# Optimization experiments

Measured on AMD Instinct MI355X. Metric: run time of the kernel, lower is better.

Reference implementation:

```python
import jax, jax.numpy as jnp
import numpy as np

INV_SQRT2 = 0.7071067811865476  # Haar (db1) filter coefficient


def _haar_wavedec(x, level):
    """Haar (db1) multi-level DWT along axis=2 of x: [B,H,L,Dh].
    Returns [cA_n, cD_n, cD_{n-1}, ..., cD_1] (pywt.wavedec ordering).
    Exact match to pywt for L divisible by 2**level (no boundary padding needed)."""
    details = []
    a = x
    for _ in range(level):
        e, o = a[:, :, 0::2, :], a[:, :, 1::2, :]
        details.append((e - o) * INV_SQRT2)
        a = (e + o) * INV_SQRT2
    return [a] + details[::-1]


def _haar_idwt_step(a, d):
    """Single-level Haar inverse DWT along axis=2."""
    e = (a + d) * INV_SQRT2
    o = (a - d) * INV_SQRT2
    B, H, Lh, Dh = a.shape
    return jnp.stack([e, o], axis=3).reshape(B, H, 2 * Lh, Dh)


def setup_inputs() -> dict:
    key = jax.random.key(0)
    ks = jax.random.split(key, 6)
    B, L, D, H, M = 8, 4096, 1024, 16, 3
    Dh = D // H
    return {
        "query": jax.random.normal(ks[0], (B, L, D), jnp.float32),
        "W_qkv": jax.random.normal(ks[1], (3 * D, D), jnp.float32) * 0.02,
        "b_qkv": jnp.zeros((3 * D,), jnp.float32),
        "W_out": jax.random.normal(ks[2], (D, D), jnp.float32) * 0.02,
        "b_out": jnp.zeros((D,), jnp.float32),
        "weight_q": jax.random.normal(ks[3], (H, M, Dh), jnp.float32),
        "weight_v": jax.random.normal(ks[4], (H, M, Dh), jnp.float32),
    }


def reference(query, W_qkv, b_qkv, W_out, b_out, weight_q, weight_v):
    B, L, D = query.shape
    H, M, Dh = weight_q.shape  # n_heads, modes, head_dim

    qkv = query @ W_qkv.T + b_qkv               # [B,L,3D]; k chunk is unused (as in original)
    q = qkv[..., :D].reshape(B, L, H, Dh).transpose(0, 2, 1, 3)      # [B,H,L,Dh]
    v = qkv[..., 2 * D:].reshape(B, L, H, Dh).transpose(0, 2, 1, 3)  # [B,H,L,Dh]

    cq = _haar_wavedec(q, M)  # [cA_M, cD_M, ..., cD_1]
    cv = _haar_wavedec(v, M)

    # Weight the coarsest `modes` bands per head/channel, then multiply q*v in wavelet domain.
    prod = []
    for j in range(M):
        wq = weight_q[None, :, j, None, :]  # [1,H,1,Dh]
        wv = weight_v[None, :, j, None, :]
        prod.append((cq[j] * wq) * (cv[j] * wv))
    prod.append(cq[M] * cv[M])  # finest detail band, unweighted

    # Inverse DWT back to length L.
    a = prod[0]
    for d in prod[1:]:
        a = _haar_idwt_step(a, d)

    out = a.transpose(0, 2, 1, 3).reshape(B, L, D)
    return out @ W_out.T + b_out  # dropout is identity in eval
```

## Files before the change

kernel.cpp:

```cpp
#include <hip/hip_runtime.h>
#include <hip/hip_fp16.h>
#include <cstdint>
#include <cstddef>

typedef _Float16 f16;
typedef __attribute__((ext_vector_type(4))) _Float16 f16x4;
typedef __attribute__((ext_vector_type(8))) _Float16 f16x8;
typedef __attribute__((ext_vector_type(4))) float f32x4;

#define C_INV_SQRT2 0.70710678118654752440f

__device__ __forceinline__ void gld_lds16(const void* g, void* l) {
  __builtin_amdgcn_global_load_lds((const __attribute__((address_space(1))) void*)g,
                                   (__attribute__((address_space(3))) void*)l, 16, 0, 0);
}

__global__ __launch_bounds__(256) void cvt_f32_f16_k(const float* __restrict__ in,
                                                     f16* __restrict__ out, int n4) {
  int i = blockIdx.x * 256 + threadIdx.x;
  if (i >= n4) return;
  const float4 x = ((const float4*)in)[i];
  f16x4 y;
  y.x = (f16)x.x; y.y = (f16)x.y; y.z = (f16)x.z; y.w = (f16)x.w;
  ((f16x4*)out)[i] = y;
}

__global__ __launch_bounds__(256) void pack_wqv_k(const float* __restrict__ W,
                                                  const float* __restrict__ b,
                                                  f16* __restrict__ Wo,
                                                  float* __restrict__ bo) {
  int i = blockIdx.x * 256 + threadIdx.x;
  int n = i >> 8;
  int c = (i & 255) * 4;
  int sn = (n < 1024) ? n : (n + 1024);
  const float4 x = *(const float4*)(W + (size_t)sn * 1024 + c);
  f16x4 y; y.x = (f16)x.x; y.y = (f16)x.y; y.z = (f16)x.z; y.w = (f16)x.w;
  *(f16x4*)(Wo + (size_t)n * 1024 + c) = y;
  if (i < 2048) bo[i] = b[(i < 1024) ? i : (i + 1024)];
}

__device__ __forceinline__ void haar_mid(const f16x8 q8, const f16x8 v8,
                                         float wq0, float wq1, float wq2,
                                         float wv0, float wv1, float wv2,
                                         float* a8) {
  const float c = C_INV_SQRT2;
  float q[8], v[8];
#pragma unroll
  for (int i = 0; i < 8; i++) { q[i] = (float)q8[i]; v[i] = (float)v8[i]; }
  float qa1[4], qd1[4], va1[4], vd1[4];
#pragma unroll
  for (int i = 0; i < 4; i++) {
    qd1[i] = (q[2 * i] - q[2 * i + 1]) * c;
    qa1[i] = (q[2 * i] + q[2 * i + 1]) * c;
    vd1[i] = (v[2 * i] - v[2 * i + 1]) * c;
    va1[i] = (v[2 * i] + v[2 * i + 1]) * c;
  }
  float qa2[2], qd2[2], va2[2], vd2[2];
#pragma unroll
  for (int j = 0; j < 2; j++) {
    qd2[j] = (qa1[2 * j] - qa1[2 * j + 1]) * c;
    qa2[j] = (qa1[2 * j] + qa1[2 * j + 1]) * c;
    vd2[j] = (va1[2 * j] - va1[2 * j + 1]) * c;
    va2[j] = (va1[2 * j] + va1[2 * j + 1]) * c;
  }
  const float qd3 = (qa2[0] - qa2[1]) * c, qa3 = (qa2[0] + qa2[1]) * c;
  const float vd3 = (va2[0] - va2[1]) * c, va3 = (va2[0] + va2[1]) * c;
  const float pa = (qa3 * wq0) * (va3 * wv0);
  const float pd3 = (qd3 * wq1) * (vd3 * wv1);
  float pd2[2], pd1[4];
#pragma unroll
  for (int j = 0; j < 2; j++) pd2[j] = (qd2[j] * wq2) * (vd2[j] * wv2);
#pragma unroll
  for (int i = 0; i < 4; i++) pd1[i] = qd1[i] * vd1[i];
  float s2[2], s1[4];
  s2[0] = (pa + pd3) * c;
  s2[1] = (pa - pd3) * c;
#pragma unroll
  for (int j = 0; j < 2; j++) {
    s1[2 * j] = (s2[j] + pd2[j]) * c;
    s1[2 * j + 1] = (s2[j] - pd2[j]) * c;
  }
#pragma unroll
  for (int i = 0; i < 4; i++) {
    a8[2 * i] = (s1[i] + pd1[i]) * c;
    a8[2 * i + 1] = (s1[i] - pd1[i]) * c;
  }
}


#define STAGEH(bufi, mat, half, Gbase, k0)                         \
  {                                                                \
    f16* Ld = &lds[bufi][mat][half][0];                            \
    const f16* Gp = (Gbase) + (size_t)srow * K + (k0) + sch * 8;   \
    gld_lds16(Gp, Ld + (w * 64) * 8);                              \
    gld_lds16(Gp + (size_t)64 * K, Ld + (4096 + w * 64 * 8));      \
  }

#define MFMA_PH(mi0)                                                             \
  __builtin_amdgcn_s_setprio(1);                                                 \
  _Pragma("unroll") for (int mm = (mi0); mm < (mi0) + 2; mm++)                   \
      _Pragma("unroll") for (int nj = 0; nj < 4; nj++) {                         \
    acc[mm][nj] = __builtin_amdgcn_mfma_f32_16x16x32_f16(aF[mm][0], bF[nj][0],   \
                                                         acc[mm][nj], 0, 0, 0);  \
    acc[mm][nj] = __builtin_amdgcn_mfma_f32_16x16x32_f16(aF[mm][1], bF[nj][1],   \
                                                         acc[mm][nj], 0, 0, 0);  \
  }                                                                              \
  __builtin_amdgcn_s_setprio(0);

#define BAR_SEQ()                       \
  __builtin_amdgcn_sched_barrier(0);    \
  __builtin_amdgcn_s_barrier();         \
  __builtin_amdgcn_sched_barrier(0);

template <typename CT, bool FUSED>
__global__ __launch_bounds__(512, 2) void gemm256_k(const f16* __restrict__ A,
                                                    const f16* __restrict__ B,
                                                    const float* __restrict__ bias,
                                                    CT* __restrict__ C,
                                                    const float* __restrict__ wq,
                                                    const float* __restrict__ wv,
                                                    int M, int N, int K, int nbx) {
  __shared__ f16 lds[2][2][2][128 * 64];
  const int t = threadIdx.x;
  const int w = t >> 6, l = t & 63;
  const int wm = w >> 2, wn = w & 3;
  const int hi = l >> 4, lo = l & 15;

  const int nwg = gridDim.x;
  const int cpx = nwg >> 3;
  const int bid = blockIdx.x;
  const int nid = (bid & 7) * cpx + (bid >> 3);
  const int by = nid / nbx, bx = nid - by * nbx;
  const int m0 = by * 256;
  const int n0 = bx * 256;
  const int d0 = bx * 128;

  const f16* GA = A + (size_t)m0 * K;
  const f16* GBq = FUSED ? (B + (size_t)d0 * K) : (B + (size_t)n0 * K);
  const f16* GBv = FUSED ? (B + (size_t)(1024 + d0) * K) : (GBq + (size_t)128 * K);

  const int srow = t >> 3;
  const int sch = (t & 7) ^ (srow & 7);

  const int colk0 = ((hi ^ (lo & 7)) << 3);
  const int colk1 = (((4 | hi) ^ (lo & 7)) << 3);

  f32x4 acc[8][4] = {};
  f16x8 aF[8][2], bF[4][2];
  const int NT = K >> 6;

  STAGEH(0, 0, 0, GA, 0); STAGEH(0, 0, 1, GA + (size_t)128 * K, 0);
  STAGEH(0, 1, 0, GBq, 0); STAGEH(0, 1, 1, GBv, 0);
  STAGEH(1, 0, 0, GA, 64); STAGEH(1, 0, 1, GA + (size_t)128 * K, 64);

  for (int tt = 0; tt < NT; ++tt) {
    const int buf = tt & 1;
    const f16* pA = &lds[buf][0][wm][0] + lo * 64;
    const f16* pB = &lds[buf][1][wn >> 1][0] + (wn & 1) * 4096 + lo * 64;
    const f16* pA0 = pA + colk0;
    const f16* pA1 = pA + colk1;
    const f16* pB0 = pB + colk0;
    const f16* pB1 = pB + colk1;

    if (tt < NT - 1) {
      asm volatile("s_waitcnt vmcnt(4)" ::: "memory");
    } else {
      asm volatile("s_waitcnt vmcnt(0)" ::: "memory");
    }
    BAR_SEQ();
    aF[0][0] = *(const f16x8*)(pA0 + 0 * 1024);
    aF[0][1] = *(const f16x8*)(pA1 + 0 * 1024);
    aF[1][0] = *(const f16x8*)(pA0 + 1 * 1024);
    aF[1][1] = *(const f16x8*)(pA1 + 1 * 1024);
#pragma unroll
    for (int nj = 0; nj < 4; nj++) {
      bF[nj][0] = *(const f16x8*)(pB0 + nj * 1024);
      bF[nj][1] = *(const f16x8*)(pB1 + nj * 1024);
    }
    aF[2][0] = *(const f16x8*)(pA0 + 2 * 1024);
    aF[2][1] = *(const f16x8*)(pA1 + 2 * 1024);
    aF[3][0] = *(const f16x8*)(pA0 + 3 * 1024);
    aF[3][1] = *(const f16x8*)(pA1 + 3 * 1024);
    if (tt + 1 < NT) STAGEH(buf ^ 1, 1, 0, GBq, (tt + 1) * 64);
    MFMA_PH(0);

    BAR_SEQ();
#pragma unroll
    for (int mi = 4; mi < 8; mi++) {
      aF[mi][0] = *(const f16x8*)(pA0 + mi * 1024);
      aF[mi][1] = *(const f16x8*)(pA1 + mi * 1024);
    }
    if (tt + 1 < NT) STAGEH(buf ^ 1, 1, 1, GBv, (tt + 1) * 64);
    MFMA_PH(2);

    asm volatile("s_waitcnt lgkmcnt(0)" ::: "memory");
    BAR_SEQ();
    if (tt + 2 < NT) STAGEH(buf, 0, 0, GA, (tt + 2) * 64);
    MFMA_PH(4);

    asm volatile("s_waitcnt lgkmcnt(0)" ::: "memory");
    BAR_SEQ();
    if (tt + 2 < NT) STAGEH(buf, 0, 1, GA + (size_t)128 * K, (tt + 2) * 64);
    MFMA_PH(6);
  }

  if (!FUSED) {
#pragma unroll
    for (int mi = 0; mi < 8; mi++) {
#pragma unroll
      for (int nj = 0; nj < 4; nj++) {
        const int col = n0 + wn * 64 + nj * 16 + lo;
        const float bb = bias[col];
        const size_t base = (size_t)(m0 + wm * 128 + mi * 16 + hi * 4) * N + col;
#pragma unroll
        for (int r = 0; r < 4; r++) C[base + (size_t)r * N] = (CT)(acc[mi][nj][r] + bb);
      }
    }
  } else {
    char* ctb = (char*)&lds[0][0][0][0];
#pragma unroll
    for (int mi = 0; mi < 8; mi++) {
#pragma unroll
      for (int nj = 0; nj < 4; nj++) {
        const int col = wn * 64 + nj * 16 + lo;
        const int bidx = (col < 128) ? (d0 + col) : (1024 + d0 + col - 128);
        const float bb = bias[bidx];
        f16x4 y;
#pragma unroll
        for (int r = 0; r < 4; r++) y[r] = (f16)(acc[mi][nj][r] + bb);
        const int row2 = (wm * 128 + mi * 16 + hi * 4) * 2;
        const int byte = (col * 512 + row2) ^ ((col & 7) << 4);
        *(f16x4*)(ctb + byte) = y;
      }
    }
    asm volatile("s_waitcnt lgkmcnt(0)" ::: "memory");
    __builtin_amdgcn_s_barrier();
#pragma unroll 1
    for (int p = 0; p < 8; ++p) {
      const int c = t & 127;
      const int g = p * 4 + (t >> 7);
      const int byq = (c * 512 + g * 16) ^ ((c & 7) << 4);
      const f16x8 q8 = *(const f16x8*)(ctb + byq);
      const f16x8 v8 = *(const f16x8*)(ctb + byq + 65536);
      const int d = d0 + c;
      const int wb = (d >> 6) * 192 + (d & 63);
      float a8[8];
      haar_mid(q8, v8, wq[wb], wq[wb + 64], wq[wb + 128],
               wv[wb], wv[wb + 64], wv[wb + 128], a8);
      const size_t rb = (size_t)(m0 + g * 8) * 1024 + d;
#pragma unroll
      for (int i = 0; i < 8; i++) C[rb + (size_t)i * 1024] = (CT)a8[i];
    }
  }
}

__global__ __launch_bounds__(256) void dwt_middle_k(const f16* __restrict__ qv,
                                                    const float* __restrict__ wq,
                                                    const float* __restrict__ wv,
                                                    f16* __restrict__ out) {
  const int g = blockIdx.x;
  const int d0 = threadIdx.x * 4;
  const size_t m0 = (size_t)g * 8;
  f16x4 qr[8], vr[8], o[8];
#pragma unroll
  for (int i = 0; i < 8; i++) {
    qr[i] = *(const f16x4*)(qv + (m0 + i) * 2048 + d0);
    vr[i] = *(const f16x4*)(qv + (m0 + i) * 2048 + 1024 + d0);
  }
#pragma unroll
  for (int dd = 0; dd < 4; dd++) {
    const int d = d0 + dd;
    const int wb = (d >> 6) * 192 + (d & 63);
    f16x8 q8, v8;
#pragma unroll
    for (int i = 0; i < 8; i++) { q8[i] = qr[i][dd]; v8[i] = vr[i][dd]; }
    float a8[8];
    haar_mid(q8, v8, wq[wb], wq[wb + 64], wq[wb + 128],
             wv[wb], wv[wb + 64], wv[wb + 128], a8);
#pragma unroll
    for (int i = 0; i < 8; i++) o[i][dd] = (f16)a8[i];
  }
#pragma unroll
  for (int i = 0; i < 8; i++) *(f16x4*)(out + (m0 + i) * 1024 + d0) = o[i];
}

extern "C" void kernel_launch(void* const* d_in, const int* in_sizes, int n_in,
                              void* d_out, int out_size, void* d_ws, size_t ws_size,
                              hipStream_t stream) {
  (void)in_sizes; (void)n_in; (void)out_size;
  const float* query = (const float*)d_in[0];
  const float* W_qkv = (const float*)d_in[1];
  const float* b_qkv = (const float*)d_in[2];
  const float* W_out = (const float*)d_in[3];
  const float* b_out = (const float*)d_in[4];
  const float* wq = (const float*)d_in[5];
  const float* wv = (const float*)d_in[6];
  float* out = (float*)d_out;

  char* ws = (char*)d_ws;
  f16* qf16 = (f16*)ws;
  f16* Wqv = (f16*)(ws + 67108864);
  float* bqv = (float*)(ws + 67108864 + 4194304);
  f16* Wout = (f16*)(ws + 67108864 + 4194304 + 8192);
  const size_t OFS_A = 67108864UL + 4194304 + 8192 + 2097152;
  const size_t NEED = OFS_A + 67108864UL;

  cvt_f32_f16_k<<<dim3(8388608 / 256), dim3(256), 0, stream>>>(query, qf16, 8388608);
  pack_wqv_k<<<dim3(2048), dim3(256), 0, stream>>>(W_qkv, b_qkv, Wqv, bqv);
  cvt_f32_f16_k<<<dim3(262144 / 256), dim3(256), 0, stream>>>(W_out, Wout, 262144);

  if (ws_size >= NEED) {
    f16* a_f16 = (f16*)(ws + OFS_A);
    gemm256_k<f16, true><<<dim3(8 * 128), dim3(512), 0, stream>>>(
        qf16, Wqv, bqv, a_f16, wq, wv, 32768, 1024, 1024, 8);
    gemm256_k<float, false><<<dim3(4 * 128), dim3(512), 0, stream>>>(
        a_f16, Wout, b_out, out, nullptr, nullptr, 32768, 1024, 1024, 4);
  } else {
    f16* qv = (f16*)d_out;
    f16* a_f16 = qf16;
    gemm256_k<f16, false><<<dim3(8 * 128), dim3(512), 0, stream>>>(
        qf16, Wqv, bqv, qv, nullptr, nullptr, 32768, 2048, 1024, 8);
    dwt_middle_k<<<dim3(4096), dim3(256), 0, stream>>>(qv, wq, wv, a_f16);
    gemm256_k<float, false><<<dim3(4 * 128), dim3(512), 0, stream>>>(
        a_f16, Wout, b_out, out, nullptr, nullptr, 32768, 1024, 1024, 4);
  }
}
```

Measured before the change: 263.8 us.

## Fuse fp32-to-fp16 query conversion into the QV GEMM A-operand load path

Drops the standalone query conversion kernel on the main path. The fused QV GEMM now loads fp32 query rows into registers, converts them to fp16 and writes them to LDS itself, which removes a full read of 128MB of fp32 and a 64MB fp16 write/read round trip. In exchange, A is loaded through registers instead of async global_load_lds. The loop waits for vmcnt(0) every iteration, which weakens overlap, and the extra float4 registers raise register pressure.

```diff
diff --git a/kernel.cpp b/kernel.cpp
--- a/kernel.cpp
+++ b/kernel.cpp
@@ -96,6 +96,27 @@
     gld_lds16(Gp + (size_t)64 * K, Ld + (4096 + w * 64 * 8));      \
   }
 
+#define A_ISSUE(k0)                                                          \
+  {                                                                          \
+    _Pragma("unroll") for (int sl = 0; sl < 4; sl++) {                       \
+      const float* gp = A32 + (size_t)(m0 + sl * 64 + srow) * K + (k0) + sch * 8; \
+      ar[sl][0] = *(const float4*)gp;                                        \
+      ar[sl][1] = *(const float4*)(gp + 4);                                  \
+    }                                                                        \
+  }
+
+#define A_WRITE(bufi)                                                        \
+  {                                                                          \
+    _Pragma("unroll") for (int sl = 0; sl < 4; sl++) {                       \
+      f16x8 y;                                                               \
+      _Pragma("unroll") for (int j = 0; j < 4; j++) {                        \
+        y[j] = (f16)ar[sl][0][j];                                            \
+        y[j + 4] = (f16)ar[sl][1][j];                                        \
+      }                                                                      \
+      *(f16x8*)(&lds[bufi][0][sl >> 1][0] + ((sl & 1) * 512 + t) * 8) = y;   \
+    }                                                                        \
+  }
+
 #define MFMA_PH(mi0)                                                             \
   __builtin_amdgcn_s_setprio(1);                                                 \
   _Pragma("unroll") for (int mm = (mi0); mm < (mi0) + 2; mm++)                   \
@@ -112,13 +133,14 @@
   __builtin_amdgcn_s_barrier();         \
   __builtin_amdgcn_sched_barrier(0);
 
-template <typename CT, bool FUSED>
+template <typename CT, bool FUSED, bool AF32>
 __global__ __launch_bounds__(512, 2) void gemm256_k(const f16* __restrict__ A,
                                                     const f16* __restrict__ B,
                                                     const float* __restrict__ bias,
                                                     CT* __restrict__ C,
                                                     const float* __restrict__ wq,
                                                     const float* __restrict__ wv,
+                                                    const float* __restrict__ A32,
                                                     int M, int N, int K, int nbx) {
   __shared__ f16 lds[2][2][2][128 * 64];
   const int t = threadIdx.x;
@@ -147,11 +169,19 @@
 
   f32x4 acc[8][4] = {};
   f16x8 aF[8][2], bF[4][2];
+  float4 ar[4][2];
   const int NT = K >> 6;
 
-  STAGEH(0, 0, 0, GA, 0); STAGEH(0, 0, 1, GA + (size_t)128 * K, 0);
-  STAGEH(0, 1, 0, GBq, 0); STAGEH(0, 1, 1, GBv, 0);
-  STAGEH(1, 0, 0, GA, 64); STAGEH(1, 0, 1, GA + (size_t)128 * K, 64);
+  STAGEH(0, 1, 0, GBq, 0);
+  STAGEH(0, 1, 1, GBv, 0);
+  if (AF32) {
+    A_ISSUE(0);  A_WRITE(0);
+    A_ISSUE(64); A_WRITE(1);
+    asm volatile("s_waitcnt lgkmcnt(0)" ::: "memory");
+  } else {
+    STAGEH(0, 0, 0, GA, 0); STAGEH(0, 0, 1, GA + (size_t)128 * K, 0);
+    STAGEH(1, 0, 0, GA, 64); STAGEH(1, 0, 1, GA + (size_t)128 * K, 64);
+  }
 
   for (int tt = 0; tt < NT; ++tt) {
     const int buf = tt & 1;
@@ -162,10 +192,14 @@
     const f16* pB0 = pB + colk0;
     const f16* pB1 = pB + colk1;
 
-    if (tt < NT - 1) {
-      asm volatile("s_waitcnt vmcnt(4)" ::: "memory");
+    if (AF32) {
+      asm volatile("s_waitcnt vmcnt(0)" ::: "memory");
     } else {
-      asm volatile("s_waitcnt vmcnt(0)" ::: "memory");
+      if (tt < NT - 1) {
+        asm volatile("s_waitcnt vmcnt(4)" ::: "memory");
+      } else {
+        asm volatile("s_waitcnt vmcnt(0)" ::: "memory");
+      }
     }
     BAR_SEQ();
     aF[0][0] = *(const f16x8*)(pA0 + 0 * 1024);
@@ -181,6 +215,7 @@
     aF[2][1] = *(const f16x8*)(pA1 + 2 * 1024);
     aF[3][0] = *(const f16x8*)(pA0 + 3 * 1024);
     aF[3][1] = *(const f16x8*)(pA1 + 3 * 1024);
+    if (AF32 && tt + 2 < NT) A_ISSUE((tt + 2) * 64);
     if (tt + 1 < NT) STAGEH(buf ^ 1, 1, 0, GBq, (tt + 1) * 64);
     MFMA_PH(0);
 
@@ -195,12 +230,18 @@
 
     asm volatile("s_waitcnt lgkmcnt(0)" ::: "memory");
     BAR_SEQ();
-    if (tt + 2 < NT) STAGEH(buf, 0, 0, GA, (tt + 2) * 64);
+    if (tt + 2 < NT) {
+      if (AF32) {
+        A_WRITE(buf);
+      } else {
+        STAGEH(buf, 0, 0, GA, (tt + 2) * 64);
+      }
+    }
     MFMA_PH(4);
 
     asm volatile("s_waitcnt lgkmcnt(0)" ::: "memory");
     BAR_SEQ();
-    if (tt + 2 < NT) STAGEH(buf, 0, 1, GA + (size_t)128 * K, (tt + 2) * 64);
+    if (!AF32 && tt + 2 < NT) STAGEH(buf, 0, 1, GA + (size_t)128 * K, (tt + 2) * 64);
     MFMA_PH(6);
   }
 
@@ -305,23 +346,23 @@
   const size_t OFS_A = 67108864UL + 4194304 + 8192 + 2097152;
   const size_t NEED = OFS_A + 67108864UL;
 
-  cvt_f32_f16_k<<<dim3(8388608 / 256), dim3(256), 0, stream>>>(query, qf16, 8388608);
   pack_wqv_k<<<dim3(2048), dim3(256), 0, stream>>>(W_qkv, b_qkv, Wqv, bqv);
   cvt_f32_f16_k<<<dim3(262144 / 256), dim3(256), 0, stream>>>(W_out, Wout, 262144);
 
   if (ws_size >= NEED) {
     f16* a_f16 = (f16*)(ws + OFS_A);
-    gemm256_k<f16, true><<<dim3(8 * 128), dim3(512), 0, stream>>>(
-        qf16, Wqv, bqv, a_f16, wq, wv, 32768, 1024, 1024, 8);
-    gemm256_k<float, false><<<dim3(4 * 128), dim3(512), 0, stream>>>(
-        a_f16, Wout, b_out, out, nullptr, nullptr, 32768, 1024, 1024, 4);
+    gemm256_k<f16, true, true><<<dim3(8 * 128), dim3(512), 0, stream>>>(
+        nullptr, Wqv, bqv, a_f16, wq, wv, query, 32768, 1024, 1024, 8);
+    gemm256_k<float, false, false><<<dim3(4 * 128), dim3(512), 0, stream>>>(
+        a_f16, Wout, b_out, out, nullptr, nullptr, nullptr, 32768, 1024, 1024, 4);
   } else {
+    cvt_f32_f16_k<<<dim3(8388608 / 256), dim3(256), 0, stream>>>(query, qf16, 8388608);
     f16* qv = (f16*)d_out;
     f16* a_f16 = qf16;
-    gemm256_k<f16, false><<<dim3(8 * 128), dim3(512), 0, stream>>>(
-        qf16, Wqv, bqv, qv, nullptr, nullptr, 32768, 2048, 1024, 8);
+    gemm256_k<f16, false, false><<<dim3(8 * 128), dim3(512), 0, stream>>>(
+        qf16, Wqv, bqv, qv, nullptr, nullptr, nullptr, 32768, 2048, 1024, 8);
     dwt_middle_k<<<dim3(4096), dim3(256), 0, stream>>>(qv, wq, wv, a_f16);
-    gemm256_k<float, false><<<dim3(4 * 128), dim3(512), 0, stream>>>(
-        a_f16, Wout, b_out, out, nullptr, nullptr, 32768, 1024, 1024, 4);
-  }
-}
+    gemm256_k<float, false, false><<<dim3(4 * 128), dim3(512), 0, stream>>>(
+        a_f16, Wout, b_out, out, nullptr, nullptr, nullptr, 32768, 1024, 1024, 4);
+  }
+}
```

New measurement: 431.6 us. +63.6%, slower.

## Restructure GEMM mainloop into 4-stage K=32 pipeline with new LDS swizzle

Applied to the files above, without the earlier changes.

Replaces the double-buffered K=64 mainloop, which staged A and B halves at several points per iteration, with a 4-buffer ring of K=32 slices. Each slice is loaded three stages ahead in one batch of four global-to-LDS loads. The LDS layout becomes 256x32 rows per operand with a new XOR swizzle and precomputed fragment offsets, and each step splits into two MFMA phases with a barrier between them. This aims to deepen the prefetch and hide global latency better, at the cost of twice as many barriers per unit of K and a different bank-conflict profile.

```diff
diff --git a/kernel.cpp b/kernel.cpp
--- a/kernel.cpp
+++ b/kernel.cpp
@@ -88,29 +88,15 @@
 }
 
 
-#define STAGEH(bufi, mat, half, Gbase, k0)                         \
-  {                                                                \
-    f16* Ld = &lds[bufi][mat][half][0];                            \
-    const f16* Gp = (Gbase) + (size_t)srow * K + (k0) + sch * 8;   \
-    gld_lds16(Gp, Ld + (w * 64) * 8);                              \
-    gld_lds16(Gp + (size_t)64 * K, Ld + (4096 + w * 64 * 8));      \
-  }
-
-#define MFMA_PH(mi0)                                                             \
-  __builtin_amdgcn_s_setprio(1);                                                 \
-  _Pragma("unroll") for (int mm = (mi0); mm < (mi0) + 2; mm++)                   \
-      _Pragma("unroll") for (int nj = 0; nj < 4; nj++) {                         \
-    acc[mm][nj] = __builtin_amdgcn_mfma_f32_16x16x32_f16(aF[mm][0], bF[nj][0],   \
-                                                         acc[mm][nj], 0, 0, 0);  \
-    acc[mm][nj] = __builtin_amdgcn_mfma_f32_16x16x32_f16(aF[mm][1], bF[nj][1],   \
-                                                         acc[mm][nj], 0, 0, 0);  \
-  }                                                                              \
-  __builtin_amdgcn_s_setprio(0);
-
-#define BAR_SEQ()                       \
-  __builtin_amdgcn_sched_barrier(0);    \
-  __builtin_amdgcn_s_barrier();         \
-  __builtin_amdgcn_sched_barrier(0);
+#define STAGE4(bufi, k0)                          \
+  {                                               \
+    f16* LA = &lds[bufi][0][0];                   \
+    f16* LB = &lds[bufi][1][0];                   \
+    gld_lds16(pGA0 + (k0), LA + dst0);            \
+    gld_lds16(pGA1 + (k0), LA + dst1);            \
+    gld_lds16(pGB0 + (k0), LB + dst0);            \
+    gld_lds16(pGB1 + (k0), LB + dst1);            \
+  }
 
 template <typename CT, bool FUSED>
 __global__ __launch_bounds__(512, 2) void gemm256_k(const f16* __restrict__ A,
@@ -120,7 +106,7 @@
                                                     const float* __restrict__ wq,
                                                     const float* __restrict__ wv,
                                                     int M, int N, int K, int nbx) {
-  __shared__ f16 lds[2][2][2][128 * 64];
+  __shared__ f16 lds[4][2][256 * 32];
   const int t = threadIdx.x;
   const int w = t >> 6, l = t & 63;
   const int wm = w >> 2, wn = w & 3;
@@ -139,69 +125,79 @@
   const f16* GBq = FUSED ? (B + (size_t)d0 * K) : (B + (size_t)n0 * K);
   const f16* GBv = FUSED ? (B + (size_t)(1024 + d0) * K) : (GBq + (size_t)128 * K);
 
-  const int srow = t >> 3;
-  const int sch = (t & 7) ^ (srow & 7);
-
-  const int colk0 = ((hi ^ (lo & 7)) << 3);
-  const int colk1 = (((4 | hi) ^ (lo & 7)) << 3);
+  const int srow = t >> 2;
+  const int sch = (t & 3) ^ ((t >> 3) & 3);
+  const f16* pGA0 = GA + (size_t)srow * K + sch * 8;
+  const f16* pGA1 = GA + (size_t)(128 + srow) * K + sch * 8;
+  const f16* pGB0 = GBq + (size_t)srow * K + sch * 8;
+  const f16* pGB1 = GBv + (size_t)srow * K + sch * 8;
+  const int dst0 = (0 * 512 + w * 64) * 8;
+  const int dst1 = (1 * 512 + w * 64) * 8;
+
+  int offA[8], offB[4];
+#pragma unroll
+  for (int mi = 0; mi < 8; mi++) {
+    const int r = wm * 128 + mi * 16 + lo;
+    offA[mi] = r * 32 + ((hi ^ ((r >> 1) & 3)) << 3);
+  }
+#pragma unroll
+  for (int nj = 0; nj < 4; nj++) {
+    const int r = wn * 64 + nj * 16 + lo;
+    offB[nj] = r * 32 + ((hi ^ ((r >> 1) & 3)) << 3);
+  }
 
   f32x4 acc[8][4] = {};
-  f16x8 aF[8][2], bF[4][2];
-  const int NT = K >> 6;
-
-  STAGEH(0, 0, 0, GA, 0); STAGEH(0, 0, 1, GA + (size_t)128 * K, 0);
-  STAGEH(0, 1, 0, GBq, 0); STAGEH(0, 1, 1, GBv, 0);
-  STAGEH(1, 0, 0, GA, 64); STAGEH(1, 0, 1, GA + (size_t)128 * K, 64);
-
-  for (int tt = 0; tt < NT; ++tt) {
-    const int buf = tt & 1;
-    const f16* pA = &lds[buf][0][wm][0] + lo * 64;
-    const f16* pB = &lds[buf][1][wn >> 1][0] + (wn & 1) * 4096 + lo * 64;
-    const f16* pA0 = pA + colk0;
-    const f16* pA1 = pA + colk1;
-    const f16* pB0 = pB + colk0;
-    const f16* pB1 = pB + colk1;
-
-    if (tt < NT - 1) {
+  const int NS = K >> 5;
+
+  STAGE4(0, 0);
+  STAGE4(1, 32);
+  STAGE4(2, 64);
+
+  for (int s = 0; s < NS; ++s) {
+    const int cur = s & 3;
+    if (s <= NS - 3) {
+      asm volatile("s_waitcnt vmcnt(8)" ::: "memory");
+    } else if (s == NS - 2) {
       asm volatile("s_waitcnt vmcnt(4)" ::: "memory");
     } else {
       asm volatile("s_waitcnt vmcnt(0)" ::: "memory");
     }
-    BAR_SEQ();
-    aF[0][0] = *(const f16x8*)(pA0 + 0 * 1024);
-    aF[0][1] = *(const f16x8*)(pA1 + 0 * 1024);
-    aF[1][0] = *(const f16x8*)(pA0 + 1 * 1024);
-    aF[1][1] = *(const f16x8*)(pA1 + 1 * 1024);
-#pragma unroll
-    for (int nj = 0; nj < 4; nj++) {
-      bF[nj][0] = *(const f16x8*)(pB0 + nj * 1024);
-      bF[nj][1] = *(const f16x8*)(pB1 + nj * 1024);
-    }
-    aF[2][0] = *(const f16x8*)(pA0 + 2 * 1024);
-    aF[2][1] = *(const f16x8*)(pA1 + 2 * 1024);
-    aF[3][0] = *(const f16x8*)(pA0 + 3 * 1024);
-    aF[3][1] = *(const f16x8*)(pA1 + 3 * 1024);
-    if (tt + 1 < NT) STAGEH(buf ^ 1, 1, 0, GBq, (tt + 1) * 64);
-    MFMA_PH(0);
-
-    BAR_SEQ();
-#pragma unroll
-    for (int mi = 4; mi < 8; mi++) {
-      aF[mi][0] = *(const f16x8*)(pA0 + mi * 1024);
-      aF[mi][1] = *(const f16x8*)(pA1 + mi * 1024);
-    }
-    if (tt + 1 < NT) STAGEH(buf ^ 1, 1, 1, GBv, (tt + 1) * 64);
-    MFMA_PH(2);
-
+    __builtin_amdgcn_sched_barrier(0);
+    __builtin_amdgcn_s_barrier();
+    __builtin_amdgcn_sched_barrier(0);
+
+    if (s + 3 < NS) STAGE4((s + 3) & 3, (s + 3) * 32);
+
+    const f16* pA = &lds[cur][0][0];
+    const f16* pB = &lds[cur][1][0];
+    f16x8 bF[4], aLo[4], aHi[4];
+#pragma unroll
+    for (int nj = 0; nj < 4; nj++) bF[nj] = *(const f16x8*)(pB + offB[nj]);
+#pragma unroll
+    for (int mi = 0; mi < 4; mi++) aLo[mi] = *(const f16x8*)(pA + offA[mi]);
+    __builtin_amdgcn_s_setprio(1);
+#pragma unroll
+    for (int mi = 0; mi < 4; mi++)
+#pragma unroll
+      for (int nj = 0; nj < 4; nj++)
+        acc[mi][nj] =
+            __builtin_amdgcn_mfma_f32_16x16x32_f16(aLo[mi], bF[nj], acc[mi][nj], 0, 0, 0);
+    __builtin_amdgcn_s_setprio(0);
+#pragma unroll
+    for (int mi = 0; mi < 4; mi++) aHi[mi] = *(const f16x8*)(pA + offA[mi + 4]);
+    __builtin_amdgcn_sched_barrier(0);
+
+    __builtin_amdgcn_s_barrier();
     asm volatile("s_waitcnt lgkmcnt(0)" ::: "memory");
-    BAR_SEQ();
-    if (tt + 2 < NT) STAGEH(buf, 0, 0, GA, (tt + 2) * 64);
-    MFMA_PH(4);
-
-    asm volatile("s_waitcnt lgkmcnt(0)" ::: "memory");
-    BAR_SEQ();
-    if (tt + 2 < NT) STAGEH(buf, 0, 1, GA + (size_t)128 * K, (tt + 2) * 64);
-    MFMA_PH(6);
+    __builtin_amdgcn_sched_barrier(0);
+    __builtin_amdgcn_s_setprio(1);
+#pragma unroll
+    for (int mi = 0; mi < 4; mi++)
+#pragma unroll
+      for (int nj = 0; nj < 4; nj++)
+        acc[mi + 4][nj] = __builtin_amdgcn_mfma_f32_16x16x32_f16(aHi[mi], bF[nj],
+                                                                 acc[mi + 4][nj], 0, 0, 0);
+    __builtin_amdgcn_s_setprio(0);
   }
 
   if (!FUSED) {
@@ -217,7 +213,8 @@
       }
     }
   } else {
-    char* ctb = (char*)&lds[0][0][0][0];
+    char* ctb = (char*)&lds[0][0][0];
+    __builtin_amdgcn_s_barrier();
 #pragma unroll
     for (int mi = 0; mi < 8; mi++) {
 #pragma unroll
```

Result: slower. 274.2 us (+3.9%).
